# Kernel tuning notes

Measured on AMD Instinct MI355X. Metric: run time of the kernel, lower is better.

The kernel has to match this reference:

```python
import jax, jax.numpy as jnp
import numpy as np

NUM_EXPERTS = 16
TOP_K = 2
Z_LOSS = 1e-3
USAGE_EMA_TAU = 1000.0


def setup_inputs() -> dict:
    key = jax.random.key(0)
    k1, k2 = jax.random.split(key)
    wm_state = jax.random.normal(k1, (4, 4096, 2048), dtype=jnp.float32)
    prototypes = jax.random.normal(k2, (NUM_EXPERTS, 1), dtype=jnp.float32)
    usage_ema = jnp.zeros((NUM_EXPERTS,), dtype=jnp.float32)
    return {"wm_state": wm_state, "prototypes": prototypes, "usage_ema": usage_ema}


def reference(wm_state, prototypes, usage_ema):
    # x = mean of the whole working-memory state -> scalar
    x = jnp.mean(wm_state)
    # negative squared distance to each 1-d prototype -> [E]
    sim = -jnp.square(prototypes[:, 0] - x)
    probs = jax.nn.softmax(sim, axis=-1)
    topk_vals, topk_idx = jax.lax.top_k(probs, TOP_K)
    # scatter ones at top-k positions
    mask = jnp.zeros_like(probs).at[topk_idx].set(1.0)
    # EMA usage update (mask is detached in the original)
    alpha = 1.0 / max(float(USAGE_EMA_TAU), 1.0)
    new_usage_ema = (1.0 - alpha) * usage_ema + alpha * jax.lax.stop_gradient(mask)
    target = 1.0 / NUM_EXPERTS
    usage_balance = jnp.mean(jnp.square(new_usage_ema - target))
    balance_loss = usage_balance * Z_LOSS
    return (mask, probs, balance_loss, new_usage_ema, topk_idx)
```

## Files before the change

### kernel.cpp

```cpp
#include <hip/hip_runtime.h>


#define NUM_EXPERTS 16
#define RED_BLOCKS 2048
#define RED_THREADS 256

__global__ __launch_bounds__(RED_THREADS)
void gw_reduce_partial(const float* __restrict__ x, double* __restrict__ partials, int n4) {
    __shared__ double sdata[RED_THREADS / 64];
    const int tid = blockIdx.x * blockDim.x + threadIdx.x;
    const int stride = gridDim.x * blockDim.x;
    const float4* __restrict__ x4 = (const float4*)x;

    double acc = 0.0;
    for (int i = tid; i < n4; i += stride) {
        float4 v = x4[i];
        acc += (double)v.x + (double)v.y + (double)v.z + (double)v.w;
    }
    #pragma unroll
    for (int off = 32; off > 0; off >>= 1)
        acc += __shfl_down(acc, off, 64);

    const int lane = threadIdx.x & 63;
    const int wave = threadIdx.x >> 6;
    if (lane == 0) sdata[wave] = acc;
    __syncthreads();
    if (threadIdx.x == 0) {
        double s = 0.0;
        #pragma unroll
        for (int w = 0; w < RED_THREADS / 64; ++w) s += sdata[w];
        partials[blockIdx.x] = s;
    }
}

__global__ __launch_bounds__(64)
void gw_finalize(const double* __restrict__ partials,
                 const float* __restrict__ prototypes,
                 const float* __restrict__ usage_ema,
                 float* __restrict__ out,
                 long long n_total) {
    double acc = 0.0;
    for (int i = threadIdx.x; i < RED_BLOCKS; i += 64) acc += partials[i];
    #pragma unroll
    for (int off = 32; off > 0; off >>= 1)
        acc += __shfl_down(acc, off, 64);

    if (threadIdx.x == 0) {
        const float x = (float)(acc / (double)n_total);

        float sim[NUM_EXPERTS];
        float m = -1e30f;
        #pragma unroll
        for (int e = 0; e < NUM_EXPERTS; ++e) {
            float d = prototypes[e] - x;
            sim[e] = -d * d;
            m = fmaxf(m, sim[e]);
        }
        float probs[NUM_EXPERTS];
        float s = 0.0f;
        #pragma unroll
        for (int e = 0; e < NUM_EXPERTS; ++e) {
            probs[e] = expf(sim[e] - m);
            s += probs[e];
        }
        const float inv_s = 1.0f / s;
        #pragma unroll
        for (int e = 0; e < NUM_EXPERTS; ++e) probs[e] *= inv_s;

        int i0 = 0;
        #pragma unroll
        for (int e = 1; e < NUM_EXPERTS; ++e)
            if (probs[e] > probs[i0]) i0 = e;
        int i1 = -1;
        #pragma unroll
        for (int e = 0; e < NUM_EXPERTS; ++e) {
            if (e == i0) continue;
            if (i1 < 0 || probs[e] > probs[i1]) i1 = e;
        }

        const float alpha = 1.0f / 1000.0f;
        const float target = 1.0f / (float)NUM_EXPERTS;
        float bal = 0.0f;
        #pragma unroll
        for (int e = 0; e < NUM_EXPERTS; ++e) {
            float mk = (e == i0 || e == i1) ? 1.0f : 0.0f;
            float ne = (1.0f - alpha) * usage_ema[e] + alpha * mk;
            out[e]      = mk;
            out[16 + e] = probs[e];
            out[33 + e] = ne;
            float dlt = ne - target;
            bal += dlt * dlt;
        }
        out[32] = (bal / (float)NUM_EXPERTS) * 1e-3f;
        out[49] = (float)i0;
        out[50] = (float)i1;
    }
}

extern "C" void kernel_launch(void* const* d_in, const int* in_sizes, int n_in,
                              void* d_out, int out_size, void* d_ws, size_t ws_size,
                              hipStream_t stream) {
    const float* wm_state   = (const float*)d_in[0];
    const float* prototypes = (const float*)d_in[1];
    const float* usage_ema  = (const float*)d_in[2];
    float* out = (float*)d_out;

    const long long n_total = (long long)in_sizes[0];
    const int n4 = (int)(n_total / 4);

    double* partials = (double*)d_ws;

    gw_reduce_partial<<<RED_BLOCKS, RED_THREADS, 0, stream>>>(wm_state, partials, n4);
    gw_finalize<<<1, 64, 0, stream>>>(partials, prototypes, usage_ema, out, n_total);
}
```

Baseline: 203.1 us.

## Fuse reduction and router finalize via last-block atomic counter, float accumulators

Result: slower. 238.3 us (+17.3%).

```diff
diff --git a/kernel.cpp b/kernel.cpp
--- a/kernel.cpp
+++ b/kernel.cpp
@@ -5,18 +5,35 @@
 #define RED_BLOCKS 2048
 #define RED_THREADS 256
 
+typedef float f32x4 __attribute__((ext_vector_type(4)));
+
 __global__ __launch_bounds__(RED_THREADS)
-void gw_reduce_partial(const float* __restrict__ x, double* __restrict__ partials, int n4) {
+void gw_router_fused(const f32x4* __restrict__ x4, int n4,
+                     const float* __restrict__ prototypes,
+                     const float* __restrict__ usage_ema,
+                     float* __restrict__ out,
+                     double* __restrict__ partials,
+                     unsigned int* __restrict__ counter,
+                     long long n_total) {
     __shared__ double sdata[RED_THREADS / 64];
+    __shared__ int s_is_last;
+
     const int tid = blockIdx.x * blockDim.x + threadIdx.x;
     const int stride = gridDim.x * blockDim.x;
-    const float4* __restrict__ x4 = (const float4*)x;
 
-    double acc = 0.0;
-    for (int i = tid; i < n4; i += stride) {
-        float4 v = x4[i];
-        acc += (double)v.x + (double)v.y + (double)v.z + (double)v.w;
+    float a0 = 0.f, a1 = 0.f, a2 = 0.f, a3 = 0.f;
+    const int iters = n4 / stride;
+    int i = tid;
+    for (int k = 0; k < iters; ++k, i += stride) {
+        f32x4 v = __builtin_nontemporal_load(x4 + i);
+        a0 += v.x; a1 += v.y; a2 += v.z; a3 += v.w;
     }
+    for (; i < n4; i += stride) {
+        f32x4 v = __builtin_nontemporal_load(x4 + i);
+        a0 += v.x; a1 += v.y; a2 += v.z; a3 += v.w;
+    }
+
+    double acc = ((double)a0 + (double)a1) + ((double)a2 + (double)a3);
     #pragma unroll
     for (int off = 32; off > 0; off >>= 1)
         acc += __shfl_down(acc, off, 64);
@@ -25,28 +42,30 @@
     const int wave = threadIdx.x >> 6;
     if (lane == 0) sdata[wave] = acc;
     __syncthreads();
+
     if (threadIdx.x == 0) {
-        double s = 0.0;
-        #pragma unroll
-        for (int w = 0; w < RED_THREADS / 64; ++w) s += sdata[w];
+        double s = sdata[0] + sdata[1] + sdata[2] + sdata[3];
         partials[blockIdx.x] = s;
+        unsigned prev = __hip_atomic_fetch_add(counter, 1u, __ATOMIC_ACQ_REL,
+                                               __HIP_MEMORY_SCOPE_AGENT);
+        s_is_last = (prev == (unsigned)(gridDim.x - 1)) ? 1 : 0;
     }
-}
+    __syncthreads();
+    if (!s_is_last) return;
 
-__global__ __launch_bounds__(64)
-void gw_finalize(const double* __restrict__ partials,
-                 const float* __restrict__ prototypes,
-                 const float* __restrict__ usage_ema,
-                 float* __restrict__ out,
-                 long long n_total) {
-    double acc = 0.0;
-    for (int i = threadIdx.x; i < RED_BLOCKS; i += 64) acc += partials[i];
+    double facc = 0.0;
+    for (int p = threadIdx.x; p < RED_BLOCKS; p += RED_THREADS)
+        facc += __hip_atomic_load(&partials[p], __ATOMIC_ACQUIRE,
+                                  __HIP_MEMORY_SCOPE_AGENT);
     #pragma unroll
     for (int off = 32; off > 0; off >>= 1)
-        acc += __shfl_down(acc, off, 64);
+        facc += __shfl_down(facc, off, 64);
+    if (lane == 0) sdata[wave] = facc;
+    __syncthreads();
 
     if (threadIdx.x == 0) {
-        const float x = (float)(acc / (double)n_total);
+        const double total = sdata[0] + sdata[1] + sdata[2] + sdata[3];
+        const float x = (float)(total / (double)n_total);
 
         float sim[NUM_EXPERTS];
         float m = -1e30f;
@@ -100,7 +119,7 @@
 extern "C" void kernel_launch(void* const* d_in, const int* in_sizes, int n_in,
                               void* d_out, int out_size, void* d_ws, size_t ws_size,
                               hipStream_t stream) {
-    const float* wm_state   = (const float*)d_in[0];
+    const f32x4* wm_state   = (const f32x4*)d_in[0];
     const float* prototypes = (const float*)d_in[1];
     const float* usage_ema  = (const float*)d_in[2];
     float* out = (float*)d_out;
@@ -109,7 +128,9 @@
     const int n4 = (int)(n_total / 4);
 
     double* partials = (double*)d_ws;
+    unsigned int* counter = (unsigned int*)((char*)d_ws + RED_BLOCKS * sizeof(double));
 
-    gw_reduce_partial<<<RED_BLOCKS, RED_THREADS, 0, stream>>>(wm_state, partials, n4);
-    gw_finalize<<<1, 64, 0, stream>>>(partials, prototypes, usage_ema, out, n_total);
+    hipMemsetAsync(counter, 0, sizeof(unsigned int), stream);
+    gw_router_fused<<<RED_BLOCKS, RED_THREADS, 0, stream>>>(
+        wm_state, n4, prototypes, usage_ema, out, partials, counter, n_total);
 }
```
